# Performance work log

Hardware: AMD Instinct MI355X
Metric: run time of the kernel (lower is better)

## Reference

```python
import jax, jax.numpy as jnp
import numpy as np

MAX_STEPS = 64      # fixed iteration budget for the adaptive loop (jit-friendly)
RTOL = 1e-5
ATOL = 1e-6


def _gru_cell_fn(Wih, bih, bhh):
    """Returns f(t, y) = d y / dt, the TemporalODERNN forward.

    PyTorch GRU with zero initial hidden state: the W_hh @ h term vanishes,
    only the hidden biases b_hh survive. Gate order in torch is [r, z, n].
    """
    H = bhh.shape[0] // 3
    br, bz, bn = bhh[:H], bhh[H:2 * H], bhh[2 * H:]

    def f(t, y):
        B = y.shape[0]
        t_col = jnp.broadcast_to(jnp.asarray(t, y.dtype), (B, 1))
        xt = jnp.concatenate([y, t_col], axis=1)          # [B, H+1]
        g = xt @ Wih.T + bih                               # [B, 3H]
        gr, gz, gn = g[:, :H], g[:, H:2 * H], g[:, 2 * H:]
        r = jax.nn.sigmoid(gr + br)
        z = jax.nn.sigmoid(gz + bz)
        n = jnp.tanh(gn + r * bn)
        return (1.0 - z) * n                               # h0 = 0 -> h' = (1-z)*n

    return f


def _dopri5_step(f, t, y, dt):
    """One Dormand-Prince 5(4) step. Returns (y_next, error_estimate)."""
    k1 = f(t, y)
    k2 = f(t + dt * 0.2, y + dt * 0.2 * k1)
    k3 = f(t + dt * 0.3, y + dt * (3 / 40 * k1 + 9 / 40 * k2))
    k4 = f(t + dt * 0.8, y + dt * (44 / 45 * k1 - 56 / 15 * k2 + 32 / 9 * k3))
    k5 = f(t + dt * (8 / 9), y + dt * (19372 / 6561 * k1 - 25360 / 2187 * k2
                                       + 64448 / 6561 * k3 - 212 / 729 * k4))
    k6 = f(t + dt, y + dt * (9017 / 3168 * k1 - 355 / 33 * k2 + 46732 / 5247 * k3
                             + 49 / 176 * k4 - 5103 / 18656 * k5))
    y5 = y + dt * (35 / 384 * k1 + 500 / 1113 * k3 + 125 / 192 * k4
                   - 2187 / 6784 * k5 + 11 / 84 * k6)
    k7 = f(t + dt, y5)
    err = dt * (71 / 57600 * k1 - 71 / 16695 * k3 + 71 / 1920 * k4
                - 17253 / 339200 * k5 + 22 / 525 * k6 - 1 / 40 * k7)
    return y5, err


def _odeint_dopri5(f, y0, t0, t1):
    """Adaptive dopri5 from t0 to t1 with a fixed iteration budget (lax.scan)."""
    dt0 = (t1 - t0) * 0.01 + 1e-8

    def body(carry, _):
        t, dt, y = carry
        done = (t1 - t) <= 1e-6
        dt_c = jnp.minimum(dt, t1 - t)                     # don't overshoot t1
        y_new, err = _dopri5_step(f, t, y, dt_c)
        scale = ATOL + RTOL * jnp.maximum(jnp.abs(y), jnp.abs(y_new))
        err_norm = jnp.sqrt(jnp.mean((err / scale) ** 2))
        accept = err_norm <= 1.0
        factor = jnp.clip(0.9 * (err_norm + 1e-10) ** (-0.2), 0.2, 10.0)
        t_n = jnp.where(accept, t + dt_c, t)
        y_n = jnp.where(accept, y_new, y)
        dt_n = dt_c * factor
        # freeze state once integration has reached t1
        return (jnp.where(done, t, t_n),
                jnp.where(done, dt, dt_n),
                jnp.where(done, y, y_n)), None

    (tf, dtf, yT), _ = jax.lax.scan(body, (t0, dt0, y0), None, length=MAX_STEPS)
    return yT


def setup_inputs() -> dict:
    key = jax.random.key(0)
    ks = jax.random.split(key, 9)
    B, D_IN, H, L = 512, 128, 256, 64
    s_p = 1.0 / np.sqrt(D_IN)
    s_g = 1.0 / np.sqrt(H)
    return {
        "x": jax.random.normal(ks[0], (B, D_IN), jnp.float32),
        "time_points": jnp.arange(8, dtype=jnp.float32),
        "Wp": jax.random.uniform(ks[1], (H, D_IN), jnp.float32, -s_p, s_p),
        "bp": jax.random.uniform(ks[2], (H,), jnp.float32, -s_p, s_p),
        "Wih": jax.random.uniform(ks[3], (3 * H, H + 1), jnp.float32, -s_g, s_g),
        "bih": jax.random.uniform(ks[4], (3 * H,), jnp.float32, -s_g, s_g),
        "Whh": jax.random.uniform(ks[5], (3 * H, H), jnp.float32, -s_g, s_g),
        "bhh": jax.random.uniform(ks[6], (3 * H,), jnp.float32, -s_g, s_g),
        "Wl": jax.random.uniform(ks[7], (L, H), jnp.float32, -s_g, s_g),
        "bl": jax.random.uniform(ks[8], (L,), jnp.float32, -s_g, s_g),
    }


def reference(x, time_points, Wp, bp, Wih, bih, Whh, bhh, Wl, bl):
    h0 = x @ Wp.T + bp                                     # input_proj: [B, H]
    f = _gru_cell_fn(Wih, bih, bhh)                        # Whh unused: h0_gru = 0
    hT = _odeint_dopri5(f, h0, time_points[0], time_points[-1])
    return hT @ Wl.T + bl                                  # latent_proj: [B, L]
```

## Files before the change

### kernel.cpp

```cpp
#include <hip/hip_runtime.h>
#include <math.h>


typedef __attribute__((ext_vector_type(8))) short bf16x8s;
typedef __attribute__((ext_vector_type(4))) float f32x4;

#define F(x) ((float)(x))
#define GLDS 4096
#define REDF 5696
#define SBF 5712
#define SWZ(b) ((b) ^ ((((b) >> 8) & 7) << 4))

static __device__ __forceinline__ unsigned short f2bf(float f) {
  unsigned u = __float_as_uint(f);
  unsigned r = (u + 0x7FFFu + ((u >> 16) & 1u)) >> 16;
  return (unsigned short)r;
}
static __device__ __forceinline__ float bf2f(unsigned short b) {
  return __uint_as_float(((unsigned)b) << 16);
}
static __device__ __forceinline__ float sigm(float x) {
  return 1.0f / (1.0f + __expf(-x));
}
static __device__ __forceinline__ float tanh_fast(float x) {
  float e = __expf(-2.0f * fabsf(x));
  float t = (1.0f - e) / (1.0f + e);
  return copysignf(t, x);
}
static __device__ __forceinline__ void pub64(unsigned long long* p,
                                             unsigned long long v) {
  __hip_atomic_store(p, v, __ATOMIC_RELAXED, __HIP_MEMORY_SCOPE_AGENT);
}
static __device__ __forceinline__ unsigned long long ld64(
    const unsigned long long* p) {
  return __hip_atomic_load(p, __ATOMIC_RELAXED, __HIP_MEMORY_SCOPE_AGENT);
}

__global__ void prep_kernel(const float* __restrict__ Wih,
                            const float* __restrict__ Wp,
                            const float* __restrict__ Wl,
                            float* __restrict__ ws) {
  int i = blockIdx.x * blockDim.x + threadIdx.x;
  if (i < 196608) {
    const int j = i & 7, l = (i >> 3) & 63, ks = (i >> 9) & 7, nt = i >> 12;
    const int c = nt * 16 + (l & 15);
    const int k = ks * 32 + (l >> 4) * 8 + j;
    const float f = Wih[c * 257 + k];
    unsigned short hi = f2bf(f);
    unsigned short lo = f2bf(f - bf2f(hi));
    ((unsigned short*)ws)[i] = hi;
    ((unsigned short*)ws)[196608 + i] = lo;
  } else if (i < 229376) {
    int ii = i - 196608; int hh = ii & 255, k = ii >> 8;
    ws[i] = Wp[hh * 128 + k];
  } else if (i < 245760) {
    int ii = i - 229376; int c = ii & 63, k = ii >> 6;
    ws[i] = Wl[c * 256 + k];
  }
}

__device__ __forceinline__ void eval_front(
    float* __restrict__ smem, unsigned long long* __restrict__ kpk,
    const bf16x8s (&bhr)[8], const bf16x8s (&blr)[8],
    int rg, int sub, int lane, int w, int fo0, int fo1, int t, int ec,
    const float (&ys)[8], float ts_,
    float cr0, float cz0, float bn_, float wtr, float wtz, float wtn,
    float bhn, float& ks_out) {
  unsigned short h_[8], l_[8];
#pragma unroll
  for (int c = 0; c < 8; ++c) {
    h_[c] = f2bf(ys[c]);
    l_[c] = f2bf(ys[c] - bf2f(h_[c]));
  }
  char* yB = (char*)smem;
  *(ushort4*)(yB + SWZ(2 * fo0)) = make_ushort4(h_[0], h_[1], h_[2], h_[3]);
  *(ushort4*)(yB + SWZ(2 * fo1)) = make_ushort4(h_[4], h_[5], h_[6], h_[7]);
  *(ushort4*)(yB + 8192 + SWZ(2 * fo0)) = make_ushort4(l_[0], l_[1], l_[2], l_[3]);
  *(ushort4*)(yB + 8192 + SWZ(2 * fo1)) = make_ushort4(l_[4], l_[5], l_[6], l_[7]);
  __syncthreads();

  if (w < 6) {
    f32x4 ac = {0.f, 0.f, 0.f, 0.f};
#pragma unroll
    for (int ks2 = 0; ks2 < 8; ++ks2) {
      const int rb = SWZ(16 * (ks2 * 64 + lane));
      const bf16x8s ah = *(const bf16x8s*)(yB + rb);
      const bf16x8s al = *(const bf16x8s*)(yB + 8192 + rb);
      ac = __builtin_amdgcn_mfma_f32_16x16x32_bf16(al, bhr[ks2], ac, 0, 0, 0);
      ac = __builtin_amdgcn_mfma_f32_16x16x32_bf16(ah, blr[ks2], ac, 0, 0, 0);
      ac = __builtin_amdgcn_mfma_f32_16x16x32_bf16(ah, bhr[ks2], ac, 0, 0, 0);
    }
    const int gcol = w * 16 + (lane & 15);
    const int gr0 = (lane >> 4) * 4;
#pragma unroll
    for (int j = 0; j < 4; ++j) smem[GLDS + (gr0 + j) * 100 + gcol] = ac[j];
  }
  __syncthreads();

  {
    const int row = t >> 5, hl = t & 31;
    const float gR = smem[GLDS + row * 100 + hl];
    const float gZ = smem[GLDS + row * 100 + 32 + hl];
    const float gN = smem[GLDS + row * 100 + 64 + hl];
    const float rv = sigm(gR + cr0 + ts_ * wtr);
    const float zv = sigm(gZ + cz0 + ts_ * wtz);
    const float nv = tanh_fast(gN + bn_ + ts_ * wtn + rv * bhn);
    const float kv = (1.0f - zv) * nv;
    ks_out = kv;
    pub64(kpk + ((size_t)((ec & 1) * 32 + rg) * 8 + sub) * 512 + row * 32 + hl,
          ((unsigned long long)(unsigned)(ec + 1) << 32) | __float_as_uint(kv));
  }
}

__device__ __forceinline__ void eval_poll(
    const unsigned long long* __restrict__ kpk,
    int rg, int w, int h0, int ec, float (&kout)[8]) {
  const int subsrc = h0 >> 5;
  const unsigned long long* kb =
      kpk + ((size_t)((ec & 1) * 32 + rg) * 8 + subsrc) * 512 + (h0 & 31);
  const unsigned tag = (unsigned)(ec + 1);
  unsigned long long q[8];
  for (;;) {
    bool ok = true;
#pragma unroll
    for (int i = 0; i < 8; ++i) {
      const int rr = (i >> 2) * 8 + w;
      q[i] = ld64(kb + rr * 32 + (i & 3));
      ok &= ((unsigned)(q[i] >> 32) == tag);
    }
    if (ok) break;
    __builtin_amdgcn_s_sleep(1);
  }
#pragma unroll
  for (int i = 0; i < 8; ++i) kout[i] = __uint_as_float((unsigned)q[i]);
}

#define EVAL(KOUT, KS, TS)                                                     \
  do {                                                                         \
    eval_front(smem, kpk, bhr, blr, rg, sub, lane, w, fo0, fo1, t, ec, ys,     \
               (TS), cr0, cz0, bn_, wtr, wtz, wtn, bhn, KS);                   \
    eval_poll(kpk, rg, w, h0, ec, KOUT);                                       \
    ++ec;                                                                      \
  } while (0)

__global__ void __launch_bounds__(512)
ode_pk(const float* __restrict__ x,
       const float* __restrict__ tp, int nt,
       const float* __restrict__ bp,
       const float* __restrict__ Wih,
       const float* __restrict__ bih,
       const float* __restrict__ bhh,
       const float* __restrict__ bl,
       const float* __restrict__ ws_f,
       unsigned long long* __restrict__ kpk,
       unsigned long long* __restrict__ ppk,
       float* __restrict__ out) {
  extern __shared__ float smem[];

  const int bid = blockIdx.x;
  const int rg = bid & 31;
  const int sub = bid >> 5;
  const int t = threadIdx.x;
  const int lane = t & 63;
  const int w = t >> 6;
  const int h0 = lane * 4;
  const int fo0 = ((h0 >> 5) * 64 + w + ((h0 >> 3) & 3) * 16) * 8 + (h0 & 7);
  const int fo1 = ((h0 >> 5) * 64 + (w + 8) + ((h0 >> 3) & 3) * 16) * 8 + (h0 & 7);

  const unsigned short* wbh = (const unsigned short*)ws_f;
  const unsigned short* wbl = ((const unsigned short*)ws_f) + 196608;
  const float* Wpt = ws_f + 196608;
  const float* Wlt = ws_f + 229376;

  const float t0 = tp[0];
  const float t1v = tp[nt - 1];

  bf16x8s bhr[8], blr[8];
  if (w < 6) {
    const int ntg = (w >> 1) * 16 + sub * 2 + (w & 1);
#pragma unroll
    for (int ks2 = 0; ks2 < 8; ++ks2) {
      bhr[ks2] = *(const bf16x8s*)(wbh + ((ntg * 8 + ks2) * 64 + lane) * 8);
      blr[ks2] = *(const bf16x8s*)(wbl + ((ntg * 8 + ks2) * 64 + lane) * 8);
    }
  } else {
#pragma unroll
    for (int ks2 = 0; ks2 < 8; ++ks2) {
      bhr[ks2] = bf16x8s{0, 0, 0, 0, 0, 0, 0, 0};
      blr[ks2] = bf16x8s{0, 0, 0, 0, 0, 0, 0, 0};
    }
  }

  const int gh = sub * 32 + (t & 31);
  const float cr0 = bih[gh] + bhh[gh];
  const float cz0 = bih[256 + gh] + bhh[256 + gh];
  const float bn_ = bih[512 + gh];
  const float bhn = bhh[512 + gh];
  const float wtr = Wih[gh * 257 + 256];
  const float wtz = Wih[(256 + gh) * 257 + 256];
  const float wtn = Wih[(512 + gh) * 257 + 256];

  for (int i = t; i < 2048; i += 512)
    smem[i] = x[(rg * 16 + (i >> 7)) * 128 + (i & 127)];
  __syncthreads();

  float yb[8];
  {
    float acc[8] = {0.f, 0.f, 0.f, 0.f, 0.f, 0.f, 0.f, 0.f};
    for (int k = 0; k < 128; ++k) {
      const float xv0 = smem[w * 128 + k];
      const float xv1 = smem[(w + 8) * 128 + k];
      const float4 wv4 = *(const float4*)(Wpt + k * 256 + h0);
      acc[0] = fmaf(xv0, wv4.x, acc[0]);
      acc[1] = fmaf(xv0, wv4.y, acc[1]);
      acc[2] = fmaf(xv0, wv4.z, acc[2]);
      acc[3] = fmaf(xv0, wv4.w, acc[3]);
      acc[4] = fmaf(xv1, wv4.x, acc[4]);
      acc[5] = fmaf(xv1, wv4.y, acc[5]);
      acc[6] = fmaf(xv1, wv4.z, acc[6]);
      acc[7] = fmaf(xv1, wv4.w, acc[7]);
    }
    const float4 bp4 = *(const float4*)(bp + h0);
    yb[0] = acc[0] + bp4.x; yb[1] = acc[1] + bp4.y;
    yb[2] = acc[2] + bp4.z; yb[3] = acc[3] + bp4.w;
    yb[4] = acc[4] + bp4.x; yb[5] = acc[5] + bp4.y;
    yb[6] = acc[6] + bp4.z; yb[7] = acc[7] + bp4.w;
  }
  float ybs;
  {
    const int row_s = t >> 5;
    float accs = 0.f;
    for (int k = 0; k < 128; ++k)
      accs = fmaf(smem[row_s * 128 + k], Wpt[k * 256 + gh], accs);
    ybs = accs + bp[gh];
  }
  __syncthreads();

  float tcur = t0;
  float dt = (t1v - t0) * 0.01f + 1e-8f;
  int ec = 0;

  float k1v[8], k2v[8], k3v[8], k4v[8], k5v[8], k6v[8], k7v[8];
  float ys[8];
  float k1s, k2s, k3s, k4s, k5s, k6s, k7s;

#pragma unroll
  for (int c = 0; c < 8; ++c) ys[c] = yb[c];
  EVAL(k1v, k1s, t0);

  for (int step = 0; step < 64; ++step) {
    if (t1v - tcur <= 1e-6f) break;
    const float dtc = fminf(dt, t1v - tcur);

#pragma unroll
    for (int c = 0; c < 8; ++c) ys[c] = fmaf(dtc * 0.2f, k1v[c], yb[c]);
    EVAL(k2v, k2s, tcur + dtc * 0.2f);

#pragma unroll
    for (int c = 0; c < 8; ++c)
      ys[c] = fmaf(dtc, fmaf(F(9.0/40.0), k2v[c], F(3.0/40.0) * k1v[c]), yb[c]);
    EVAL(k3v, k3s, tcur + dtc * 0.3f);

#pragma unroll
    for (int c = 0; c < 8; ++c) {
      float in_ = F(44.0/45.0) * k1v[c];
      in_ = fmaf(F(-56.0/15.0), k2v[c], in_);
      in_ = fmaf(F(32.0/9.0), k3v[c], in_);
      ys[c] = fmaf(dtc, in_, yb[c]);
    }
    EVAL(k4v, k4s, tcur + dtc * 0.8f);

#pragma unroll
    for (int c = 0; c < 8; ++c) {
      float in_ = F(19372.0/6561.0) * k1v[c];
      in_ = fmaf(F(-25360.0/2187.0), k2v[c], in_);
      in_ = fmaf(F(64448.0/6561.0), k3v[c], in_);
      in_ = fmaf(F(-212.0/729.0), k4v[c], in_);
      ys[c] = fmaf(dtc, in_, yb[c]);
    }
    EVAL(k5v, k5s, tcur + dtc * F(8.0/9.0));

#pragma unroll
    for (int c = 0; c < 8; ++c) {
      float in_ = F(9017.0/3168.0) * k1v[c];
      in_ = fmaf(F(-355.0/33.0), k2v[c], in_);
      in_ = fmaf(F(46732.0/5247.0), k3v[c], in_);
      in_ = fmaf(F(49.0/176.0), k4v[c], in_);
      in_ = fmaf(F(-5103.0/18656.0), k5v[c], in_);
      ys[c] = fmaf(dtc, in_, yb[c]);
    }
    EVAL(k6v, k6s, tcur + dtc);

#pragma unroll
    for (int c = 0; c < 8; ++c) {
      float in_ = F(35.0/384.0) * k1v[c];
      in_ = fmaf(F(500.0/1113.0), k3v[c], in_);
      in_ = fmaf(F(125.0/192.0), k4v[c], in_);
      in_ = fmaf(F(-2187.0/6784.0), k5v[c], in_);
      in_ = fmaf(F(11.0/84.0), k6v[c], in_);
      ys[c] = fmaf(dtc, in_, yb[c]);
    }
    eval_front(smem, kpk, bhr, blr, rg, sub, lane, w, fo0, fo1, t, ec, ys,
               tcur + dtc, cr0, cz0, bn_, wtr, wtz, wtn, bhn, k7s);

    float y5s;
    {
      float in_ = F(35.0/384.0) * k1s;
      in_ = fmaf(F(500.0/1113.0), k3s, in_);
      in_ = fmaf(F(125.0/192.0), k4s, in_);
      in_ = fmaf(F(-2187.0/6784.0), k5s, in_);
      in_ = fmaf(F(11.0/84.0), k6s, in_);
      y5s = fmaf(dtc, in_, ybs);
    }
    double lsum;
    {
      float ev = F(71.0/57600.0) * k1s;
      ev = fmaf(F(-71.0/16695.0), k3s, ev);
      ev = fmaf(F(71.0/1920.0), k4s, ev);
      ev = fmaf(F(-17253.0/339200.0), k5s, ev);
      ev = fmaf(F(22.0/525.0), k6s, ev);
      ev = fmaf(F(-1.0/40.0), k7s, ev);
      ev *= dtc;
      const float sc = 1e-6f + 1e-5f * fmaxf(fabsf(ybs), fabsf(y5s));
      const float qq = ev / sc;
      lsum = (double)(qq * qq);
    }
    double v = lsum;
#pragma unroll
    for (int d = 1; d < 64; d <<= 1) v += __shfl_xor(v, d, 64);
    if (lane == 0) ((double*)(smem + REDF))[w] = v;
    __syncthreads();
    if (t == 0) {
      double s = ((double*)(smem + REDF))[0];
#pragma unroll
      for (int i = 1; i < 8; ++i) s += ((double*)(smem + REDF))[i];
      const unsigned long long bits =
          (unsigned long long)__double_as_longlong(s);
      const unsigned long long tg =
          ((unsigned long long)(unsigned)(step + 1)) << 32;
      unsigned long long* pb = ppk + ((size_t)((step & 1) * 32 + rg) * 8 + sub) * 2;
      pub64(pb + 0, tg | (unsigned)(bits & 0xffffffffull));
      pub64(pb + 1, tg | (unsigned)(bits >> 32));
    }
    eval_poll(kpk, rg, w, h0, ec, k7v);
    ++ec;
    __syncthreads();

    double myp = 0.0;
    if (t < 256) {
      const int prg = t >> 3, psub = t & 7;
      const unsigned long long* pb =
          ppk + ((size_t)((step & 1) * 32 + prg) * 8 + psub) * 2;
      const unsigned tg = (unsigned)(step + 1);
      unsigned long long a, b;
      for (;;) {
        a = ld64(pb + 0);
        b = ld64(pb + 1);
        if (((unsigned)(a >> 32) == tg) && ((unsigned)(b >> 32) == tg)) break;
        __builtin_amdgcn_s_sleep(1);
      }
      myp = __longlong_as_double(
          (long long)(((unsigned long long)(unsigned)b << 32) |
                      (unsigned)(a & 0xffffffffull)));
    }
    double v3 = myp;
#pragma unroll
    for (int d = 1; d < 64; d <<= 1) v3 += __shfl_xor(v3, d, 64);
    if (lane == 0) ((double*)(smem + REDF))[w] = v3;
    __syncthreads();
    if (t == 0) {
      double s = ((double*)(smem + REDF))[0];
#pragma unroll
      for (int i = 1; i < 8; ++i) s += ((double*)(smem + REDF))[i];
      ((double*)(smem + SBF))[0] = s;
    }
    __syncthreads();
    const double sb = ((double*)(smem + SBF))[0];
    const float err_norm = sqrtf((float)(sb / 131072.0));
    const bool accept = (err_norm <= 1.0f);
    float factor = 0.9f * powf(err_norm + 1e-10f, -0.2f);
    factor = fminf(10.0f, fmaxf(0.2f, factor));
    if (accept) {
      tcur = tcur + dtc;
#pragma unroll
      for (int c = 0; c < 8; ++c) { yb[c] = ys[c]; k1v[c] = k7v[c]; }
      ybs = y5s; k1s = k7s;
    }
    dt = dtc * factor;
  }

  __syncthreads();
#pragma unroll
  for (int c = 0; c < 4; ++c) {
    smem[w * 256 + h0 + c] = yb[c];
    smem[(w + 8) * 256 + h0 + c] = yb[4 + c];
  }
  __syncthreads();
  if (sub == 0) {
    const int oc = t & 63;
#pragma unroll
    for (int rr = 0; rr < 2; ++rr) {
      const int orow = (t >> 6) + rr * 8;
      float acc = bl[oc];
      for (int k = 0; k < 256; ++k)
        acc = fmaf(smem[orow * 256 + k], Wlt[k * 64 + oc], acc);
      out[(rg * 16 + orow) * 64 + oc] = acc;
    }
  }
}

extern "C" void kernel_launch(void* const* d_in, const int* in_sizes, int n_in,
                              void* d_out, int out_size, void* d_ws, size_t ws_size,
                              hipStream_t stream) {
  const float* x   = (const float*)d_in[0];
  const float* tp  = (const float*)d_in[1];
  const float* Wp  = (const float*)d_in[2];
  const float* bp  = (const float*)d_in[3];
  const float* Wih = (const float*)d_in[4];
  const float* bih = (const float*)d_in[5];
  const float* bhh = (const float*)d_in[7];
  const float* Wl  = (const float*)d_in[8];
  const float* bl  = (const float*)d_in[9];
  float* out = (float*)d_out;
  float* ws_f = (float*)d_ws;
  unsigned long long* kpk = (unsigned long long*)((char*)d_ws + 1048576);
  unsigned long long* ppk = (unsigned long long*)((char*)d_ws + 3145728);
  int nt = in_sizes[1];

  hipLaunchKernelGGL(prep_kernel, dim3(960), dim3(256), 0, stream, Wih, Wp, Wl, ws_f);
  hipMemsetAsync((char*)d_ws + 1048576, 0, 2105344, stream);

  const size_t shbytes = 23040;
  hipFuncSetAttribute((const void*)ode_pk,
                      hipFuncAttributeMaxDynamicSharedMemorySize, (int)shbytes);

  void* args[] = { (void*)&x, (void*)&tp, (void*)&nt, (void*)&bp, (void*)&Wih,
                   (void*)&bih, (void*)&bhh, (void*)&bl, (void*)&ws_f,
                   (void*)&kpk, (void*)&ppk, (void*)&out };
  hipLaunchCooperativeKernel((void*)ode_pk, dim3(256), dim3(512), args,
                             shbytes, stream);
}
```

Measured before the change: 299.8 us.

## Repartition ODE solve to 128 blocks of 1024 threads, stage RK stages in LDS

The cooperative grid shrinks from 256 blocks of 512 threads to 128 blocks of 1024 threads. Each block now owns 64 hidden units instead of 32, and 12 of its waves run MFMA instead of 6. Each thread handles one batch row rather than two, and the seven Runge-Kutta stage vectors move from registers into a large LDS buffer. The aim is to halve the number of blocks that publish and poll through global memory at each stage, and to cut register pressure. In exchange, LDS use grows to about 140KB per block, and the polled k-values are shared through LDS traffic.

Result: slower. 401.1 us (+33.8%).

```diff
diff --git a/kernel.cpp b/kernel.cpp
--- a/kernel.cpp
+++ b/kernel.cpp
@@ -6,9 +6,10 @@
 typedef __attribute__((ext_vector_type(4))) float f32x4;
 
 #define F(x) ((float)(x))
-#define GLDS 4096
-#define REDF 5696
-#define SBF 5712
+#define GOFF 4096
+#define KOFF 7232
+#define REDF 35904
+#define SBF 35936
 #define SWZ(b) ((b) ^ ((((b) >> 8) & 7) << 4))
 
 static __device__ __forceinline__ unsigned short f2bf(float f) {
@@ -62,24 +63,22 @@
 __device__ __forceinline__ void eval_front(
     float* __restrict__ smem, unsigned long long* __restrict__ kpk,
     const bf16x8s (&bhr)[8], const bf16x8s (&blr)[8],
-    int rg, int sub, int lane, int w, int fo0, int fo1, int t, int ec,
-    const float (&ys)[8], float ts_,
+    int rg, int sub, int lane, int w, int fo, int t, int ec,
+    const float (&ys)[4], float ts_,
     float cr0, float cz0, float bn_, float wtr, float wtz, float wtn,
     float bhn, float& ks_out) {
-  unsigned short h_[8], l_[8];
-#pragma unroll
-  for (int c = 0; c < 8; ++c) {
+  unsigned short h_[4], l_[4];
+#pragma unroll
+  for (int c = 0; c < 4; ++c) {
     h_[c] = f2bf(ys[c]);
     l_[c] = f2bf(ys[c] - bf2f(h_[c]));
   }
   char* yB = (char*)smem;
-  *(ushort4*)(yB + SWZ(2 * fo0)) = make_ushort4(h_[0], h_[1], h_[2], h_[3]);
-  *(ushort4*)(yB + SWZ(2 * fo1)) = make_ushort4(h_[4], h_[5], h_[6], h_[7]);
-  *(ushort4*)(yB + 8192 + SWZ(2 * fo0)) = make_ushort4(l_[0], l_[1], l_[2], l_[3]);
-  *(ushort4*)(yB + 8192 + SWZ(2 * fo1)) = make_ushort4(l_[4], l_[5], l_[6], l_[7]);
-  __syncthreads();
-
-  if (w < 6) {
+  *(ushort4*)(yB + SWZ(2 * fo)) = make_ushort4(h_[0], h_[1], h_[2], h_[3]);
+  *(ushort4*)(yB + 8192 + SWZ(2 * fo)) = make_ushort4(l_[0], l_[1], l_[2], l_[3]);
+  __syncthreads();
+
+  if (w < 12) {
     f32x4 ac = {0.f, 0.f, 0.f, 0.f};
 #pragma unroll
     for (int ks2 = 0; ks2 < 8; ++ks2) {
@@ -90,71 +89,73 @@
       ac = __builtin_amdgcn_mfma_f32_16x16x32_bf16(ah, blr[ks2], ac, 0, 0, 0);
       ac = __builtin_amdgcn_mfma_f32_16x16x32_bf16(ah, bhr[ks2], ac, 0, 0, 0);
     }
-    const int gcol = w * 16 + (lane & 15);
+    const int gcol = (w >> 2) * 64 + (w & 3) * 16 + (lane & 15);
     const int gr0 = (lane >> 4) * 4;
 #pragma unroll
-    for (int j = 0; j < 4; ++j) smem[GLDS + (gr0 + j) * 100 + gcol] = ac[j];
+    for (int j = 0; j < 4; ++j) smem[GOFF + (gr0 + j) * 196 + gcol] = ac[j];
   }
   __syncthreads();
 
   {
-    const int row = t >> 5, hl = t & 31;
-    const float gR = smem[GLDS + row * 100 + hl];
-    const float gZ = smem[GLDS + row * 100 + 32 + hl];
-    const float gN = smem[GLDS + row * 100 + 64 + hl];
+    const int row = t >> 6, hl = t & 63;
+    const float gR = smem[GOFF + row * 196 + hl];
+    const float gZ = smem[GOFF + row * 196 + 64 + hl];
+    const float gN = smem[GOFF + row * 196 + 128 + hl];
     const float rv = sigm(gR + cr0 + ts_ * wtr);
     const float zv = sigm(gZ + cz0 + ts_ * wtz);
     const float nv = tanh_fast(gN + bn_ + ts_ * wtn + rv * bhn);
     const float kv = (1.0f - zv) * nv;
     ks_out = kv;
-    pub64(kpk + ((size_t)((ec & 1) * 32 + rg) * 8 + sub) * 512 + row * 32 + hl,
+    pub64(kpk + ((size_t)((ec & 1) * 128 + rg * 4 + sub)) * 1024 + t,
           ((unsigned long long)(unsigned)(ec + 1) << 32) | __float_as_uint(kv));
   }
 }
 
 __device__ __forceinline__ void eval_poll(
-    const unsigned long long* __restrict__ kpk,
-    int rg, int w, int h0, int ec, float (&kout)[8]) {
-  const int subsrc = h0 >> 5;
+    float* __restrict__ smem, const unsigned long long* __restrict__ kpk,
+    int rg, int w, int lane, int h0, int ec, int slot) {
   const unsigned long long* kb =
-      kpk + ((size_t)((ec & 1) * 32 + rg) * 8 + subsrc) * 512 + (h0 & 31);
+      kpk + ((size_t)((ec & 1) * 128 + rg * 4 + (lane >> 4))) * 1024 +
+      w * 64 + (h0 & 63);
   const unsigned tag = (unsigned)(ec + 1);
-  unsigned long long q[8];
+  unsigned long long q[4];
   for (;;) {
     bool ok = true;
 #pragma unroll
-    for (int i = 0; i < 8; ++i) {
-      const int rr = (i >> 2) * 8 + w;
-      q[i] = ld64(kb + rr * 32 + (i & 3));
+    for (int i = 0; i < 4; ++i) {
+      q[i] = ld64(kb + i);
       ok &= ((unsigned)(q[i] >> 32) == tag);
     }
     if (ok) break;
     __builtin_amdgcn_s_sleep(1);
   }
-#pragma unroll
-  for (int i = 0; i < 8; ++i) kout[i] = __uint_as_float((unsigned)q[i]);
-}
-
-#define EVAL(KOUT, KS, TS)                                                     \
+  *(float4*)(smem + KOFF + slot * 4096 + w * 256 + h0) =
+      make_float4(__uint_as_float((unsigned)q[0]), __uint_as_float((unsigned)q[1]),
+                  __uint_as_float((unsigned)q[2]), __uint_as_float((unsigned)q[3]));
+}
+
+#define KH(i) (*(const float4*)(smem + KOFF + (i) * 4096 + w * 256 + h0))
+
+#define EVAL(SLOT, KS, TS)                                                     \
   do {                                                                         \
-    eval_front(smem, kpk, bhr, blr, rg, sub, lane, w, fo0, fo1, t, ec, ys,     \
-               (TS), cr0, cz0, bn_, wtr, wtz, wtn, bhn, KS);                   \
-    eval_poll(kpk, rg, w, h0, ec, KOUT);                                       \
+    eval_front(smem, kpk, bhr, blr, rg, sub, lane, w, fo, t, ec, ys, (TS),     \
+               cr0, cz0, bn_, wtr, wtz, wtn, bhn, KS);                         \
+    eval_poll(smem, kpk, rg, w, lane, h0, ec, SLOT);                           \
     ++ec;                                                                      \
   } while (0)
 
-__global__ void __launch_bounds__(512)
-ode_pk(const float* __restrict__ x,
-       const float* __restrict__ tp, int nt,
-       const float* __restrict__ bp,
-       const float* __restrict__ Wih,
-       const float* __restrict__ bih,
-       const float* __restrict__ bhh,
-       const float* __restrict__ bl,
-       const float* __restrict__ ws_f,
-       unsigned long long* __restrict__ kpk,
-       unsigned long long* __restrict__ ppk,
-       float* __restrict__ out) {
+__global__ void __launch_bounds__(1024, 1)
+ode_pk4(const float* __restrict__ x,
+        const float* __restrict__ tp, int nt,
+        const float* __restrict__ bp,
+        const float* __restrict__ Wih,
+        const float* __restrict__ bih,
+        const float* __restrict__ bhh,
+        const float* __restrict__ bl,
+        const float* __restrict__ ws_f,
+        unsigned long long* __restrict__ kpk,
+        unsigned long long* __restrict__ ppk,
+        float* __restrict__ out) {
   extern __shared__ float smem[];
 
   const int bid = blockIdx.x;
@@ -164,8 +165,7 @@
   const int lane = t & 63;
   const int w = t >> 6;
   const int h0 = lane * 4;
-  const int fo0 = ((h0 >> 5) * 64 + w + ((h0 >> 3) & 3) * 16) * 8 + (h0 & 7);
-  const int fo1 = ((h0 >> 5) * 64 + (w + 8) + ((h0 >> 3) & 3) * 16) * 8 + (h0 & 7);
+  const int fo = ((h0 >> 5) * 64 + w + ((h0 >> 3) & 3) * 16) * 8 + (h0 & 7);
 
   const unsigned short* wbh = (const unsigned short*)ws_f;
   const unsigned short* wbl = ((const unsigned short*)ws_f) + 196608;
@@ -176,8 +176,8 @@
   const float t1v = tp[nt - 1];
 
   bf16x8s bhr[8], blr[8];
-  if (w < 6) {
-    const int ntg = (w >> 1) * 16 + sub * 2 + (w & 1);
+  if (w < 12) {
+    const int ntg = (w >> 2) * 16 + sub * 4 + (w & 3);
 #pragma unroll
     for (int ks2 = 0; ks2 < 8; ++ks2) {
       bhr[ks2] = *(const bf16x8s*)(wbh + ((ntg * 8 + ks2) * 64 + lane) * 8);
@@ -191,7 +191,7 @@
     }
   }
 
-  const int gh = sub * 32 + (t & 31);
+  const int gh = sub * 64 + (t & 63);
   const float cr0 = bih[gh] + bhh[gh];
   const float cz0 = bih[256 + gh] + bhh[256 + gh];
   const float bn_ = bih[512 + gh];
@@ -200,35 +200,28 @@
   const float wtz = Wih[(256 + gh) * 257 + 256];
   const float wtn = Wih[(512 + gh) * 257 + 256];
 
-  for (int i = t; i < 2048; i += 512)
+  for (int i = t; i < 2048; i += 1024)
     smem[i] = x[(rg * 16 + (i >> 7)) * 128 + (i & 127)];
   __syncthreads();
 
-  float yb[8];
+  float yb[4];
   {
-    float acc[8] = {0.f, 0.f, 0.f, 0.f, 0.f, 0.f, 0.f, 0.f};
+    float acc[4] = {0.f, 0.f, 0.f, 0.f};
     for (int k = 0; k < 128; ++k) {
       const float xv0 = smem[w * 128 + k];
-      const float xv1 = smem[(w + 8) * 128 + k];
       const float4 wv4 = *(const float4*)(Wpt + k * 256 + h0);
       acc[0] = fmaf(xv0, wv4.x, acc[0]);
       acc[1] = fmaf(xv0, wv4.y, acc[1]);
       acc[2] = fmaf(xv0, wv4.z, acc[2]);
       acc[3] = fmaf(xv0, wv4.w, acc[3]);
-      acc[4] = fmaf(xv1, wv4.x, acc[4]);
-      acc[5] = fmaf(xv1, wv4.y, acc[5]);
-      acc[6] = fmaf(xv1, wv4.z, acc[6]);
-      acc[7] = fmaf(xv1, wv4.w, acc[7]);
     }
     const float4 bp4 = *(const float4*)(bp + h0);
     yb[0] = acc[0] + bp4.x; yb[1] = acc[1] + bp4.y;
     yb[2] = acc[2] + bp4.z; yb[3] = acc[3] + bp4.w;
-    yb[4] = acc[4] + bp4.x; yb[5] = acc[5] + bp4.y;
-    yb[6] = acc[6] + bp4.z; yb[7] = acc[7] + bp4.w;
   }
   float ybs;
   {
-    const int row_s = t >> 5;
+    const int row_s = t >> 6;
     float accs = 0.f;
     for (int k = 0; k < 128; ++k)
       accs = fmaf(smem[row_s * 128 + k], Wpt[k * 256 + gh], accs);
@@ -240,67 +233,87 @@
   float dt = (t1v - t0) * 0.01f + 1e-8f;
   int ec = 0;
 
-  float k1v[8], k2v[8], k3v[8], k4v[8], k5v[8], k6v[8], k7v[8];
-  float ys[8];
+  float ys[4];
   float k1s, k2s, k3s, k4s, k5s, k6s, k7s;
 
 #pragma unroll
-  for (int c = 0; c < 8; ++c) ys[c] = yb[c];
-  EVAL(k1v, k1s, t0);
+  for (int c = 0; c < 4; ++c) ys[c] = yb[c];
+  EVAL(0, k1s, t0);
 
   for (int step = 0; step < 64; ++step) {
     if (t1v - tcur <= 1e-6f) break;
     const float dtc = fminf(dt, t1v - tcur);
 
-#pragma unroll
-    for (int c = 0; c < 8; ++c) ys[c] = fmaf(dtc * 0.2f, k1v[c], yb[c]);
-    EVAL(k2v, k2s, tcur + dtc * 0.2f);
-
-#pragma unroll
-    for (int c = 0; c < 8; ++c)
-      ys[c] = fmaf(dtc, fmaf(F(9.0/40.0), k2v[c], F(3.0/40.0) * k1v[c]), yb[c]);
-    EVAL(k3v, k3s, tcur + dtc * 0.3f);
-
-#pragma unroll
-    for (int c = 0; c < 8; ++c) {
-      float in_ = F(44.0/45.0) * k1v[c];
-      in_ = fmaf(F(-56.0/15.0), k2v[c], in_);
-      in_ = fmaf(F(32.0/9.0), k3v[c], in_);
-      ys[c] = fmaf(dtc, in_, yb[c]);
-    }
-    EVAL(k4v, k4s, tcur + dtc * 0.8f);
-
-#pragma unroll
-    for (int c = 0; c < 8; ++c) {
-      float in_ = F(19372.0/6561.0) * k1v[c];
-      in_ = fmaf(F(-25360.0/2187.0), k2v[c], in_);
-      in_ = fmaf(F(64448.0/6561.0), k3v[c], in_);
-      in_ = fmaf(F(-212.0/729.0), k4v[c], in_);
-      ys[c] = fmaf(dtc, in_, yb[c]);
-    }
-    EVAL(k5v, k5s, tcur + dtc * F(8.0/9.0));
-
-#pragma unroll
-    for (int c = 0; c < 8; ++c) {
-      float in_ = F(9017.0/3168.0) * k1v[c];
-      in_ = fmaf(F(-355.0/33.0), k2v[c], in_);
-      in_ = fmaf(F(46732.0/5247.0), k3v[c], in_);
-      in_ = fmaf(F(49.0/176.0), k4v[c], in_);
-      in_ = fmaf(F(-5103.0/18656.0), k5v[c], in_);
-      ys[c] = fmaf(dtc, in_, yb[c]);
-    }
-    EVAL(k6v, k6s, tcur + dtc);
-
-#pragma unroll
-    for (int c = 0; c < 8; ++c) {
-      float in_ = F(35.0/384.0) * k1v[c];
-      in_ = fmaf(F(500.0/1113.0), k3v[c], in_);
-      in_ = fmaf(F(125.0/192.0), k4v[c], in_);
-      in_ = fmaf(F(-2187.0/6784.0), k5v[c], in_);
-      in_ = fmaf(F(11.0/84.0), k6v[c], in_);
-      ys[c] = fmaf(dtc, in_, yb[c]);
-    }
-    eval_front(smem, kpk, bhr, blr, rg, sub, lane, w, fo0, fo1, t, ec, ys,
+    {
+      const float4 K1 = KH(0);
+#pragma unroll
+      for (int c = 0; c < 4; ++c) ys[c] = fmaf(dtc * 0.2f, K1[c], yb[c]);
+    }
+    EVAL(1, k2s, tcur + dtc * 0.2f);
+
+    {
+      const float4 K1 = KH(0); const float4 K2 = KH(1);
+#pragma unroll
+      for (int c = 0; c < 4; ++c)
+        ys[c] = fmaf(dtc, fmaf(F(9.0/40.0), K2[c], F(3.0/40.0) * K1[c]), yb[c]);
+    }
+    EVAL(2, k3s, tcur + dtc * 0.3f);
+
+    {
+      const float4 K1 = KH(0); const float4 K2 = KH(1); const float4 K3 = KH(2);
+#pragma unroll
+      for (int c = 0; c < 4; ++c) {
+        float in_ = F(44.0/45.0) * K1[c];
+        in_ = fmaf(F(-56.0/15.0), K2[c], in_);
+        in_ = fmaf(F(32.0/9.0), K3[c], in_);
+        ys[c] = fmaf(dtc, in_, yb[c]);
+      }
+    }
+    EVAL(3, k4s, tcur + dtc * 0.8f);
+
+    {
+      const float4 K1 = KH(0); const float4 K2 = KH(1); const float4 K3 = KH(2);
+      const float4 K4 = KH(3);
+#pragma unroll
+      for (int c = 0; c < 4; ++c) {
+        float in_ = F(19372.0/6561.0) * K1[c];
+        in_ = fmaf(F(-25360.0/2187.0), K2[c], in_);
+        in_ = fmaf(F(64448.0/6561.0), K3[c], in_);
+        in_ = fmaf(F(-212.0/729.0), K4[c], in_);
+        ys[c] = fmaf(dtc, in_, yb[c]);
+      }
+    }
+    EVAL(4, k5s, tcur + dtc * F(8.0/9.0));
+
+    {
+      const float4 K1 = KH(0); const float4 K2 = KH(1); const float4 K3 = KH(2);
+      const float4 K4 = KH(3); const float4 K5 = KH(4);
+#pragma unroll
+      for (int c = 0; c < 4; ++c) {
+        float in_ = F(9017.0/3168.0) * K1[c];
+        in_ = fmaf(F(-355.0/33.0), K2[c], in_);
+        in_ = fmaf(F(46732.0/5247.0), K3[c], in_);
+        in_ = fmaf(F(49.0/176.0), K4[c], in_);
+        in_ = fmaf(F(-5103.0/18656.0), K5[c], in_);
+        ys[c] = fmaf(dtc, in_, yb[c]);
+      }
+    }
+    EVAL(5, k6s, tcur + dtc);
+
+    {
+      const float4 K1 = KH(0); const float4 K3 = KH(2); const float4 K4 = KH(3);
+      const float4 K5 = KH(4); const float4 K6 = KH(5);
+#pragma unroll
+      for (int c = 0; c < 4; ++c) {
+        float in_ = F(35.0/384.0) * K1[c];
+        in_ = fmaf(F(500.0/1113.0), K3[c], in_);
+        in_ = fmaf(F(125.0/192.0), K4[c], in_);
+        in_ = fmaf(F(-2187.0/6784.0), K5[c], in_);
+        in_ = fmaf(F(11.0/84.0), K6[c], in_);
+        ys[c] = fmaf(dtc, in_, yb[c]);
+      }
+    }
+    eval_front(smem, kpk, bhr, blr, rg, sub, lane, w, fo, t, ec, ys,
                tcur + dtc, cr0, cz0, bn_, wtr, wtz, wtn, bhn, k7s);
 
     float y5s;
@@ -333,24 +346,24 @@
     if (t == 0) {
       double s = ((double*)(smem + REDF))[0];
 #pragma unroll
-      for (int i = 1; i < 8; ++i) s += ((double*)(smem + REDF))[i];
+      for (int i = 1; i < 16; ++i) s += ((double*)(smem + REDF))[i];
       const unsigned long long bits =
           (unsigned long long)__double_as_longlong(s);
       const unsigned long long tg =
           ((unsigned long long)(unsigned)(step + 1)) << 32;
-      unsigned long long* pb = ppk + ((size_t)((step & 1) * 32 + rg) * 8 + sub) * 2;
+      unsigned long long* pb = ppk + ((size_t)((step & 1) * 32 + rg) * 4 + sub) * 2;
       pub64(pb + 0, tg | (unsigned)(bits & 0xffffffffull));
       pub64(pb + 1, tg | (unsigned)(bits >> 32));
     }
-    eval_poll(kpk, rg, w, h0, ec, k7v);
+    eval_poll(smem, kpk, rg, w, lane, h0, ec, 6);
     ++ec;
     __syncthreads();
 
     double myp = 0.0;
-    if (t < 256) {
-      const int prg = t >> 3, psub = t & 7;
+    if (t < 128) {
+      const int prg = t >> 2, psub = t & 3;
       const unsigned long long* pb =
-          ppk + ((size_t)((step & 1) * 32 + prg) * 8 + psub) * 2;
+          ppk + ((size_t)((step & 1) * 32 + prg) * 4 + psub) * 2;
       const unsigned tg = (unsigned)(step + 1);
       unsigned long long a, b;
       for (;;) {
@@ -371,7 +384,7 @@
     if (t == 0) {
       double s = ((double*)(smem + REDF))[0];
 #pragma unroll
-      for (int i = 1; i < 8; ++i) s += ((double*)(smem + REDF))[i];
+      for (int i = 1; i < 16; ++i) s += ((double*)(smem + REDF))[i];
       ((double*)(smem + SBF))[0] = s;
     }
     __syncthreads();
@@ -383,7 +396,8 @@
     if (accept) {
       tcur = tcur + dtc;
 #pragma unroll
-      for (int c = 0; c < 8; ++c) { yb[c] = ys[c]; k1v[c] = k7v[c]; }
+      for (int c = 0; c < 4; ++c) yb[c] = ys[c];
+      *(float4*)(smem + KOFF + 0 * 4096 + w * 256 + h0) = KH(6);
       ybs = y5s; k1s = k7s;
     }
     dt = dtc * factor;
@@ -391,21 +405,14 @@
 
   __syncthreads();
 #pragma unroll
-  for (int c = 0; c < 4; ++c) {
-    smem[w * 256 + h0 + c] = yb[c];
-    smem[(w + 8) * 256 + h0 + c] = yb[4 + c];
-  }
+  for (int c = 0; c < 4; ++c) smem[w * 256 + h0 + c] = yb[c];
   __syncthreads();
   if (sub == 0) {
-    const int oc = t & 63;
-#pragma unroll
-    for (int rr = 0; rr < 2; ++rr) {
-      const int orow = (t >> 6) + rr * 8;
-      float acc = bl[oc];
-      for (int k = 0; k < 256; ++k)
-        acc = fmaf(smem[orow * 256 + k], Wlt[k * 64 + oc], acc);
-      out[(rg * 16 + orow) * 64 + oc] = acc;
-    }
+    const int orow = t >> 6, oc = t & 63;
+    float acc = bl[oc];
+    for (int k = 0; k < 256; ++k)
+      acc = fmaf(smem[orow * 256 + k], Wlt[k * 64 + oc], acc);
+    out[(rg * 16 + orow) * 64 + oc] = acc;
   }
 }
 
@@ -428,15 +435,15 @@
   int nt = in_sizes[1];
 
   hipLaunchKernelGGL(prep_kernel, dim3(960), dim3(256), 0, stream, Wih, Wp, Wl, ws_f);
-  hipMemsetAsync((char*)d_ws + 1048576, 0, 2105344, stream);
-
-  const size_t shbytes = 23040;
-  hipFuncSetAttribute((const void*)ode_pk,
+  hipMemsetAsync((char*)d_ws + 1048576, 0, 2101248, stream);
+
+  const size_t shbytes = 143808;
+  hipFuncSetAttribute((const void*)ode_pk4,
                       hipFuncAttributeMaxDynamicSharedMemorySize, (int)shbytes);
 
   void* args[] = { (void*)&x, (void*)&tp, (void*)&nt, (void*)&bp, (void*)&Wih,
                    (void*)&bih, (void*)&bhh, (void*)&bl, (void*)&ws_f,
                    (void*)&kpk, (void*)&ppk, (void*)&out };
-  hipLaunchCooperativeKernel((void*)ode_pk, dim3(256), dim3(512), args,
+  hipLaunchCooperativeKernel((void*)ode_pk4, dim3(128), dim3(1024), args,
                              shbytes, stream);
 }
```

## Remap per-thread state ownership to contiguous 8-element chunks matching MFMA layout

Applied to the files above, without the earlier changes.

Each thread now owns 8 consecutive hidden units of a single batch row instead of 4 units in each of two rows. The bf16 hi/lo staging of y into LDS becomes one 16-byte vector store per buffer, and polling of peer k values reads 8 contiguous tagged words instead of strided ones. The goal is fewer LDS store instructions and more coalesced global polling on the critical path of every stage evaluation. The ownership mapping changes for the input projection, the polling, and the final output, so they must stay consistent with the MFMA fragment layout.

New measurement: 365.0 us. 1.22x slower.

```diff
diff --git a/kernel.cpp b/kernel.cpp
--- a/kernel.cpp
+++ b/kernel.cpp
@@ -3,6 +3,7 @@
 
 
 typedef __attribute__((ext_vector_type(8))) short bf16x8s;
+typedef __attribute__((ext_vector_type(8))) unsigned short u16x8;
 typedef __attribute__((ext_vector_type(4))) float f32x4;
 
 #define F(x) ((float)(x))
@@ -62,21 +63,20 @@
 __device__ __forceinline__ void eval_front(
     float* __restrict__ smem, unsigned long long* __restrict__ kpk,
     const bf16x8s (&bhr)[8], const bf16x8s (&blr)[8],
-    int rg, int sub, int lane, int w, int fo0, int fo1, int t, int ec,
+    int rg, int sub, int lane, int w, int t, int ec,
     const float (&ys)[8], float ts_,
     float cr0, float cz0, float bn_, float wtr, float wtz, float wtn,
     float bhn, float& ks_out) {
-  unsigned short h_[8], l_[8];
+  u16x8 hv, lv;
 #pragma unroll
   for (int c = 0; c < 8; ++c) {
-    h_[c] = f2bf(ys[c]);
-    l_[c] = f2bf(ys[c] - bf2f(h_[c]));
+    const unsigned short hh = f2bf(ys[c]);
+    hv[c] = hh;
+    lv[c] = f2bf(ys[c] - bf2f(hh));
   }
   char* yB = (char*)smem;
-  *(ushort4*)(yB + SWZ(2 * fo0)) = make_ushort4(h_[0], h_[1], h_[2], h_[3]);
-  *(ushort4*)(yB + SWZ(2 * fo1)) = make_ushort4(h_[4], h_[5], h_[6], h_[7]);
-  *(ushort4*)(yB + 8192 + SWZ(2 * fo0)) = make_ushort4(l_[0], l_[1], l_[2], l_[3]);
-  *(ushort4*)(yB + 8192 + SWZ(2 * fo1)) = make_ushort4(l_[4], l_[5], l_[6], l_[7]);
+  *(u16x8*)(yB + SWZ(16 * t)) = hv;
+  *(u16x8*)(yB + 8192 + SWZ(16 * t)) = lv;
   __syncthreads();
 
   if (w < 6) {
@@ -114,18 +114,17 @@
 
 __device__ __forceinline__ void eval_poll(
     const unsigned long long* __restrict__ kpk,
-    int rg, int w, int h0, int ec, float (&kout)[8]) {
-  const int subsrc = h0 >> 5;
+    int rg, int w, int lane, int ec, float (&kout)[8]) {
   const unsigned long long* kb =
-      kpk + ((size_t)((ec & 1) * 32 + rg) * 8 + subsrc) * 512 + (h0 & 31);
+      kpk + ((size_t)((ec & 1) * 32 + rg) * 8 + w) * 512 +
+      (lane & 15) * 32 + (lane >> 4) * 8;
   const unsigned tag = (unsigned)(ec + 1);
   unsigned long long q[8];
   for (;;) {
     bool ok = true;
 #pragma unroll
     for (int i = 0; i < 8; ++i) {
-      const int rr = (i >> 2) * 8 + w;
-      q[i] = ld64(kb + rr * 32 + (i & 3));
+      q[i] = ld64(kb + i);
       ok &= ((unsigned)(q[i] >> 32) == tag);
     }
     if (ok) break;
@@ -137,9 +136,9 @@
 
 #define EVAL(KOUT, KS, TS)                                                     \
   do {                                                                         \
-    eval_front(smem, kpk, bhr, blr, rg, sub, lane, w, fo0, fo1, t, ec, ys,     \
-               (TS), cr0, cz0, bn_, wtr, wtz, wtn, bhn, KS);                   \
-    eval_poll(kpk, rg, w, h0, ec, KOUT);                                       \
+    eval_front(smem, kpk, bhr, blr, rg, sub, lane, w, t, ec, ys, (TS),         \
+               cr0, cz0, bn_, wtr, wtz, wtn, bhn, KS);                         \
+    eval_poll(kpk, rg, w, lane, ec, KOUT);                                     \
     ++ec;                                                                      \
   } while (0)
 
@@ -163,9 +162,8 @@
   const int t = threadIdx.x;
   const int lane = t & 63;
   const int w = t >> 6;
-  const int h0 = lane * 4;
-  const int fo0 = ((h0 >> 5) * 64 + w + ((h0 >> 3) & 3) * 16) * 8 + (h0 & 7);
-  const int fo1 = ((h0 >> 5) * 64 + (w + 8) + ((h0 >> 3) & 3) * 16) * 8 + (h0 & 7);
+  const int orow = lane & 15;
+  const int oh0 = w * 32 + (lane >> 4) * 8;
 
   const unsigned short* wbh = (const unsigned short*)ws_f;
   const unsigned short* wbl = ((const unsigned short*)ws_f) + 196608;
@@ -208,23 +206,24 @@
   {
     float acc[8] = {0.f, 0.f, 0.f, 0.f, 0.f, 0.f, 0.f, 0.f};
     for (int k = 0; k < 128; ++k) {
-      const float xv0 = smem[w * 128 + k];
-      const float xv1 = smem[(w + 8) * 128 + k];
-      const float4 wv4 = *(const float4*)(Wpt + k * 256 + h0);
-      acc[0] = fmaf(xv0, wv4.x, acc[0]);
-      acc[1] = fmaf(xv0, wv4.y, acc[1]);
-      acc[2] = fmaf(xv0, wv4.z, acc[2]);
-      acc[3] = fmaf(xv0, wv4.w, acc[3]);
-      acc[4] = fmaf(xv1, wv4.x, acc[4]);
-      acc[5] = fmaf(xv1, wv4.y, acc[5]);
-      acc[6] = fmaf(xv1, wv4.z, acc[6]);
-      acc[7] = fmaf(xv1, wv4.w, acc[7]);
-    }
-    const float4 bp4 = *(const float4*)(bp + h0);
-    yb[0] = acc[0] + bp4.x; yb[1] = acc[1] + bp4.y;
-    yb[2] = acc[2] + bp4.z; yb[3] = acc[3] + bp4.w;
-    yb[4] = acc[4] + bp4.x; yb[5] = acc[5] + bp4.y;
-    yb[6] = acc[6] + bp4.z; yb[7] = acc[7] + bp4.w;
+      const float xv = smem[orow * 128 + k];
+      const float4 wa = *(const float4*)(Wpt + k * 256 + oh0);
+      const float4 wb = *(const float4*)(Wpt + k * 256 + oh0 + 4);
+      acc[0] = fmaf(xv, wa.x, acc[0]);
+      acc[1] = fmaf(xv, wa.y, acc[1]);
+      acc[2] = fmaf(xv, wa.z, acc[2]);
+      acc[3] = fmaf(xv, wa.w, acc[3]);
+      acc[4] = fmaf(xv, wb.x, acc[4]);
+      acc[5] = fmaf(xv, wb.y, acc[5]);
+      acc[6] = fmaf(xv, wb.z, acc[6]);
+      acc[7] = fmaf(xv, wb.w, acc[7]);
+    }
+    const float4 ba = *(const float4*)(bp + oh0);
+    const float4 bb = *(const float4*)(bp + oh0 + 4);
+    yb[0] = acc[0] + ba.x; yb[1] = acc[1] + ba.y;
+    yb[2] = acc[2] + ba.z; yb[3] = acc[3] + ba.w;
+    yb[4] = acc[4] + bb.x; yb[5] = acc[5] + bb.y;
+    yb[6] = acc[6] + bb.z; yb[7] = acc[7] + bb.w;
   }
   float ybs;
   {
@@ -300,7 +299,7 @@
       in_ = fmaf(F(11.0/84.0), k6v[c], in_);
       ys[c] = fmaf(dtc, in_, yb[c]);
     }
-    eval_front(smem, kpk, bhr, blr, rg, sub, lane, w, fo0, fo1, t, ec, ys,
+    eval_front(smem, kpk, bhr, blr, rg, sub, lane, w, t, ec, ys,
                tcur + dtc, cr0, cz0, bn_, wtr, wtz, wtn, bhn, k7s);
 
     float y5s;
@@ -342,7 +341,7 @@
       pub64(pb + 0, tg | (unsigned)(bits & 0xffffffffull));
       pub64(pb + 1, tg | (unsigned)(bits >> 32));
     }
-    eval_poll(kpk, rg, w, h0, ec, k7v);
+    eval_poll(kpk, rg, w, lane, ec, k7v);
     ++ec;
     __syncthreads();
 
@@ -391,20 +390,17 @@
 
   __syncthreads();
 #pragma unroll
-  for (int c = 0; c < 4; ++c) {
-    smem[w * 256 + h0 + c] = yb[c];
-    smem[(w + 8) * 256 + h0 + c] = yb[4 + c];
-  }
+  for (int c = 0; c < 8; ++c) smem[orow * 256 + oh0 + c] = yb[c];
   __syncthreads();
   if (sub == 0) {
     const int oc = t & 63;
 #pragma unroll
     for (int rr = 0; rr < 2; ++rr) {
-      const int orow = (t >> 6) + rr * 8;
+      const int orw = (t >> 6) + rr * 8;
       float acc = bl[oc];
       for (int k = 0; k < 256; ++k)
-        acc = fmaf(smem[orow * 256 + k], Wlt[k * 64 + oc], acc);
-      out[(rg * 16 + orow) * 64 + oc] = acc;
+        acc = fmaf(smem[orw * 256 + k], Wlt[k * 64 + oc], acc);
+      out[(rg * 16 + orw) * 64 + oc] = acc;
     }
   }
 }
```
